# Optimization experiments

Hardware: AMD Instinct MI355X
Metric: run time of the kernel (lower is better)

Reference implementation:

```python
import jax, jax.numpy as jnp
import numpy as np

EPS = 1e-5

def _layernorm(x, w, b):
    # x: [B, L, C]; WithBias_LayerNorm over last dim (biased variance)
    mu = jnp.mean(x, axis=-1, keepdims=True)
    var = jnp.mean((x - mu) ** 2, axis=-1, keepdims=True)
    return (x - mu) / jnp.sqrt(var + EPS) * w + b

def _selective_scan(x, x_proj_w, dt_w, A_logs, Ds):
    # x: [B, D, L]  (D = ssm d_inner = 192, N = d_state = 16, R = dt_rank = 6)
    Bsz, D, L = x.shape
    N = A_logs.shape[1]
    R = dt_w.shape[1]
    x_dbl = jnp.einsum('bdl,rd->blr', x, x_proj_w)            # [B, L, R+2N]
    dts_r = x_dbl[..., :R]
    Bs = x_dbl[..., R:R + N]                                   # [B, L, N]
    Cs = x_dbl[..., R + N:]                                    # [B, L, N]
    dts = jax.nn.softplus(jnp.einsum('blr,dr->bld', dts_r, dt_w))  # [B, L, D]
    As = -jnp.exp(A_logs.astype(jnp.float32))                  # [D, N]
    dt_A = jnp.exp(jnp.einsum('bld,dn->bldn', dts, As))        # [B, L, D, N]
    dt_B_x = jnp.einsum('bld,bln,bdl->bldn', dts, Bs, x)       # [B, L, D, N]

    def step(u, inp):
        a, bx, c = inp                                         # [B,D,N],[B,D,N],[B,N]
        u = a * u + bx
        y = jnp.einsum('bdn,bn->bd', u, c)
        return u, y

    u0 = jnp.zeros((Bsz, D, N), dtype=jnp.float32)
    _, ys = jax.lax.scan(step, u0, (jnp.swapaxes(dt_A, 0, 1),
                                     jnp.swapaxes(dt_B_x, 0, 1),
                                     jnp.swapaxes(Cs, 0, 1)))
    y = jnp.swapaxes(ys, 0, 1)                                 # [B, L, D]
    y = y + jnp.einsum('bdl,d->bld', x, Ds.astype(jnp.float32))
    return y


def setup_inputs() -> dict:
    key = jax.random.key(0)
    ks = jax.random.split(key, 12)
    B, C, H, W = 64, 2048, 24, 8
    D_in2, Dssm, N, R = 384, 192, 16, 6
    s = 0.02
    return {
        'feat_map': jax.random.normal(ks[0], (B, C, H, W), jnp.float32),
        'ln_w': jnp.ones((C,), jnp.float32),
        'ln_b': jnp.zeros((C,), jnp.float32),
        'in_w': jax.random.normal(ks[1], (D_in2, C), jnp.float32) * s,
        'in_b': jnp.zeros((D_in2,), jnp.float32),
        'x_proj_w': jax.random.normal(ks[2], (R + 2 * N, Dssm), jnp.float32) * s,
        'dt_w': jax.random.normal(ks[3], (Dssm, R), jnp.float32) * 0.1,
        'A_logs': jnp.log(jnp.broadcast_to(jnp.arange(1, N + 1, dtype=jnp.float32), (Dssm, N))),
        'Ds': jnp.ones((Dssm,), jnp.float32),
        'out_w': jax.random.normal(ks[4], (C, Dssm), jnp.float32) * s,
        'out_b': jnp.zeros((C,), jnp.float32),
        'mo_w': jax.random.normal(ks[5], (C, C), jnp.float32) * s,
        'mo_b': jnp.zeros((C,), jnp.float32),
        'bn_w': jnp.ones((C,), jnp.float32),
        'bn_b': jnp.zeros((C,), jnp.float32),
        'bn_rm': jax.random.normal(ks[6], (C,), jnp.float32) * 0.1,
        'bn_rv': jax.random.uniform(ks[7], (C,), jnp.float32) + 0.5,
    }


def reference(feat_map, ln_w, ln_b, in_w, in_b, x_proj_w, dt_w, A_logs, Ds,
              out_w, out_b, mo_w, mo_b, bn_w, bn_b, bn_rm, bn_rv):
    B, C, H, W = feat_map.shape
    L = H * W
    x3 = feat_map.transpose(0, 2, 3, 1).reshape(B, L, C)       # to_3d
    fm = _layernorm(x3, ln_w, ln_b)                            # normalized feat_map [B, L, C]
    xz = jnp.einsum('blc,oc->blo', fm, in_w) + in_b            # 1x1 conv in_proj
    x, z = jnp.split(xz, 2, axis=-1)                           # each [B, L, 192]
    xd = jnp.swapaxes(x, 1, 2)                                 # [B, D, L]
    yf = _selective_scan(xd, x_proj_w, dt_w, A_logs, Ds)       # [B, L, D]
    yb = _selective_scan(xd[:, :, ::-1], x_proj_w, dt_w, A_logs, Ds)[:, ::-1, :]
    ssm = yf + yb                                              # [B, L, D]
    ssm = ssm * jax.nn.silu(z)
    out = jnp.einsum('bld,cd->blc', ssm, out_w) + out_b        # out_proj 1x1 conv
    out = out + fm                                             # drop_path is identity at eval
    out = jnp.einsum('blc,oc->blo', out, mo_w) + mo_b          # mamba_out conv 1x1
    out = (out - bn_rm) / jnp.sqrt(bn_rv + EPS) * bn_w + bn_b  # BatchNorm (eval)
    out = jax.nn.relu(out)
    return out.reshape(B, H, W, C).transpose(0, 3, 1, 2)
```

## Files before the change

kernel.cpp:

```cpp
#include <hip/hip_runtime.h>
#include <math.h>

#define EPSV 1e-5f


typedef __attribute__((ext_vector_type(8))) __bf16 bf16x8;
typedef __attribute__((ext_vector_type(4))) float f32x4;

__device__ __forceinline__ ushort f2bf(float f) {
  union { float f; unsigned u; } v; v.f = f;
  const unsigned r = v.u + 0x7fffu + ((v.u >> 16) & 1u);
  return (ushort)(r >> 16);
}

#define GLOAD16(G, L) __builtin_amdgcn_global_load_lds( \
    (__attribute__((address_space(1))) void*)(G), \
    (__attribute__((address_space(3))) void*)(L), 16, 0, 0)

#define BAR() do { asm volatile("" ::: "memory"); \
  __builtin_amdgcn_s_barrier(); \
  asm volatile("" ::: "memory"); } while (0)

template<int CTRL>
__device__ __forceinline__ float dpp_add(float y) {
  const int s = __builtin_amdgcn_update_dpp(0, __float_as_int(y), CTRL, 0xF, 0xF, true);
  return y + __int_as_float(s);
}
__device__ __forceinline__ float reduce16(float y) {
  y = dpp_add<0xB1>(y);
  y = dpp_add<0x4E>(y);
  y = dpp_add<0x124>(y);
  y = dpp_add<0x128>(y);
  return y;
}

__global__ __launch_bounds__(256) void cvt_kernel(
    const float* __restrict__ s, ushort* __restrict__ d, int n)
{
  const int i = (blockIdx.x * 256 + threadIdx.x) * 4;
  if (i + 3 < n) {
    const float4 v = *(const float4*)(s + i);
    ushort4 o;
    o.x = f2bf(v.x); o.y = f2bf(v.y); o.z = f2bf(v.z); o.w = f2bf(v.w);
    *(ushort4*)(d + i) = o;
  }
}

__global__ __launch_bounds__(256) void transpose_w(
    const float* __restrict__ w, ushort* __restrict__ wT)
{
  __shared__ float t[64][65];
  const int c0 = blockIdx.x * 64, d0 = blockIdx.y * 64;
  const int tl = threadIdx.x & 63, tg = threadIdx.x >> 6;
#pragma unroll
  for (int r = 0; r < 16; ++r) {
    const int c = r * 4 + tg;
    t[c][tl] = w[(size_t)(c0 + c) * 192 + d0 + tl];
  }
  __syncthreads();
#pragma unroll
  for (int r = 0; r < 16; ++r) {
    const int d = r * 4 + tg;
    wT[(size_t)(d0 + d) * 2048 + c0 + tl] = f2bf(t[tl][d]);
  }
}

__global__ __launch_bounds__(256) void ln_stats(
    const float* __restrict__ feat, float* __restrict__ sums)
{
  const int b = blockIdx.x, c0 = blockIdx.y * 128;
  const int l = threadIdx.x;
  if (l >= 192) return;
  const float* p = feat + ((size_t)b * 2048 + c0) * 192 + l;
  float s = 0.f, sq = 0.f;
  for (int c = 0; c < 128; ++c) { const float v = p[(size_t)c * 192]; s += v; sq = fmaf(v, v, sq); }
  atomicAdd(&sums[(b * 192 + l) * 2], s);
  atomicAdd(&sums[(b * 192 + l) * 2 + 1], sq);
}

__global__ __launch_bounds__(256) void ln_apply(
    const float* __restrict__ feat, const float* __restrict__ sums,
    const float* __restrict__ lnw, const float* __restrict__ lnb,
    ushort* __restrict__ fm)
{
  __shared__ float tile[64][65];
  __shared__ float smu[64], srs[64];
  const int b = blockIdx.x, c0 = blockIdx.y * 64, l0 = blockIdx.z * 64;
  const int tl = threadIdx.x & 63, tg = threadIdx.x >> 6;
#pragma unroll
  for (int r = 0; r < 16; ++r) {
    const int c = r * 4 + tg;
    tile[c][tl] = feat[((size_t)b * 2048 + c0 + c) * 192 + l0 + tl];
  }
  if (threadIdx.x < 64) {
    const float s  = sums[(b * 192 + l0 + threadIdx.x) * 2];
    const float sq = sums[(b * 192 + l0 + threadIdx.x) * 2 + 1];
    const float mu = s * (1.f / 2048.f);
    smu[threadIdx.x] = mu;
    srs[threadIdx.x] = rsqrtf(sq * (1.f / 2048.f) - mu * mu + EPSV);
  }
  __syncthreads();
  const float w = lnw[c0 + tl], bb = lnb[c0 + tl];
#pragma unroll
  for (int r = 0; r < 16; ++r) {
    const int ll = r * 4 + tg;
    fm[((size_t)(b * 192 + l0 + ll)) * 2048 + c0 + tl] =
        f2bf((tile[tl][ll] - smu[ll]) * srs[ll] * w + bb);
  }
}

__device__ __forceinline__ void mfma_phase(
    const ushort* __restrict__ Ag, int lda,
    const ushort* __restrict__ Bg, int ldb, int K,
    int bm, int bn, int tid, ushort* As, ushort* Bs, f32x4 acc[4][4])
{
  const int lane = tid & 63, wave = tid >> 6;
  const int wm = (wave & 1) << 6, wn = (wave >> 1) << 6;
  const int fr = lane & 15, q = lane >> 4;
  const int r0 = tid >> 2, kc = (tid & 3) << 3;
  const int lb = (tid & 192) * 8;
  for (int k0 = 0; k0 < K; k0 += 32) {
    __syncthreads();
    GLOAD16(Ag + (size_t)(bm + r0) * lda + k0 + kc,      As + lb);
    GLOAD16(Ag + (size_t)(bm + 64 + r0) * lda + k0 + kc, As + 2048 + lb);
    GLOAD16(Bg + (size_t)(bn + r0) * ldb + k0 + kc,      Bs + lb);
    GLOAD16(Bg + (size_t)(bn + 64 + r0) * ldb + k0 + kc, Bs + 2048 + lb);
    __syncthreads();
    bf16x8 af[4], bfr[4];
#pragma unroll
    for (int i = 0; i < 4; ++i) {
      af[i]  = *(const bf16x8*)&As[(wm + i * 16 + fr) * 32 + q * 8];
      bfr[i] = *(const bf16x8*)&Bs[(wn + i * 16 + fr) * 32 + q * 8];
    }
#pragma unroll
    for (int i = 0; i < 4; ++i)
#pragma unroll
      for (int j = 0; j < 4; ++j)
        acc[i][j] = __builtin_amdgcn_mfma_f32_16x16x32_bf16(af[i], bfr[j], acc[i][j], 0, 0, 0);
  }
}

__global__ __launch_bounds__(256) void mfma_gemm0(
    const ushort* __restrict__ A1, const ushort* __restrict__ B1,
    const float* __restrict__ p0, float* __restrict__ out)
{
  __shared__ ushort As[4096], Bs[4096];
  const int tid = threadIdx.x;
  const int bm = blockIdx.y * 128, bn = blockIdx.x * 128;
  f32x4 acc[4][4];
#pragma unroll
  for (int i = 0; i < 4; ++i)
#pragma unroll
    for (int j = 0; j < 4; ++j) acc[i][j] = (f32x4)(0.f);

  mfma_phase(A1, 2048, B1, 2048, 2048, bm, bn, tid, As, Bs, acc);

  const int lane = tid & 63, wave = tid >> 6;
  const int wm = (wave & 1) << 6, wn = (wave >> 1) << 6;
  const int fr = lane & 15, q = lane >> 4;
#pragma unroll
  for (int mi = 0; mi < 4; ++mi) {
    const int m0 = bm + wm + mi * 16 + q * 4;
#pragma unroll
    for (int ni = 0; ni < 4; ++ni) {
      const int n = bn + wn + ni * 16 + fr;
      const float bias = p0[n];
#pragma unroll
      for (int r = 0; r < 4; ++r)
        out[(size_t)(m0 + r) * 384 + n] = acc[mi][ni][r] + bias;
    }
  }
}

__global__ __launch_bounds__(256) void w2_partial(
    const ushort* __restrict__ A1, const ushort* __restrict__ B1,
    float* __restrict__ part)
{
  __shared__ ushort As[4096], Bs[4096];
  const int tid = threadIdx.x;
  const int bm = blockIdx.y * 128, bn = blockIdx.x * 128;
  const int kz = blockIdx.z * 256;
  f32x4 acc[4][4];
#pragma unroll
  for (int i = 0; i < 4; ++i)
#pragma unroll
    for (int j = 0; j < 4; ++j) acc[i][j] = (f32x4)(0.f);

  mfma_phase(A1 + kz, 2048, B1 + kz, 2048, 256, bm, bn, tid, As, Bs, acc);

  const int lane = tid & 63, wave = tid >> 6;
  const int wm = (wave & 1) << 6, wn = (wave >> 1) << 6;
  const int fr = lane & 15, q = lane >> 4;
  float* pout = part + (size_t)blockIdx.z * 2048 * 256;
#pragma unroll
  for (int mi = 0; mi < 4; ++mi) {
    const int m0 = bm + wm + mi * 16 + q * 4;
#pragma unroll
    for (int ni = 0; ni < 4; ++ni) {
      const int n = bn + wn + ni * 16 + fr;
#pragma unroll
      for (int r = 0; r < 4; ++r)
        pout[(size_t)(m0 + r) * 256 + n] = acc[mi][ni][r];
    }
  }
}

__global__ __launch_bounds__(256) void w2_reduce(
    const float* __restrict__ part, ushort* __restrict__ W2b)
{
  const int i = blockIdx.x * 256 + threadIdx.x;
  const float4* p4 = (const float4*)part;
  float4 s = p4[i];
#pragma unroll
  for (int z = 1; z < 8; ++z) {
    const float4 v = p4[i + z * 131072];
    s.x += v.x; s.y += v.y; s.z += v.z; s.w += v.w;
  }
  ushort4 o;
  o.x = f2bf(s.x); o.y = f2bf(s.y); o.z = f2bf(s.z); o.w = f2bf(s.w);
  *(ushort4*)(W2b + (size_t)i * 4) = o;
}

__device__ __forceinline__ void stage_half(
    int t, int kind,
    int bm, int bn, int tid,
    const ushort* __restrict__ fmw, const ushort* __restrict__ mow,
    const ushort* __restrict__ ssmb, const ushort* __restrict__ w2b,
    ushort* As, ushort* Bs)
{
  const bool isA = (kind < 2);
  const ushort* G; int ld, k0;
  if (t < 32) { G = isA ? fmw : mow;  ld = 2048; k0 = t * 64; }
  else        { G = isA ? ssmb : w2b; ld = 256;  k0 = (t - 32) * 64; }
  const int p0 = isA ? bm : bn;
  ushort* L = (isA ? As : Bs) + (t & 1) * 16384 + (kind & 1) * 8192;
  const int w = tid >> 6, l = tid & 63;
#pragma unroll
  for (int j = 0; j < 2; ++j) {
    const int LC = j * 512 + w * 64 + l;
    const int row = (kind & 1) * 128 + (LC >> 3);
    const int sc = (LC & 7) ^ (row & 7);
    GLOAD16(G + (size_t)(p0 + row) * ld + k0 + sc * 8, L + j * 4096 + w * 512);
  }
}

__global__ __launch_bounds__(512, 2) void mfma_gemm_big(
    const ushort* __restrict__ fmw,  const ushort* __restrict__ mow,
    const ushort* __restrict__ ssmb, const ushort* __restrict__ w2b,
    const float* __restrict__ scale, const float* __restrict__ shift,
    float* __restrict__ out)
{
  __shared__ ushort As[2 * 16384];
  __shared__ ushort Bs[2 * 16384];
  const int tid = threadIdx.x;
  const int flat = blockIdx.x;
  const int bx = flat & 7, by = flat >> 3;
  const int bm = by * 256, bn = bx * 256;

  const int lane = tid & 63, wave = tid >> 6;
  const int wr = wave >> 2, wc = wave & 3;
  const int fr = lane & 15, q = lane >> 4;

  constexpr int NT = 36;

  f32x4 acc[8][4];
#pragma unroll
  for (int i = 0; i < 8; ++i)
#pragma unroll
    for (int j = 0; j < 4; ++j) acc[i][j] = (f32x4)(0.f);

  stage_half(0, 0, bm, bn, tid, fmw, mow, ssmb, w2b, As, Bs);
  stage_half(0, 1, bm, bn, tid, fmw, mow, ssmb, w2b, As, Bs);
  stage_half(0, 2, bm, bn, tid, fmw, mow, ssmb, w2b, As, Bs);
  stage_half(0, 3, bm, bn, tid, fmw, mow, ssmb, w2b, As, Bs);
  stage_half(1, 2, bm, bn, tid, fmw, mow, ssmb, w2b, As, Bs);
  stage_half(1, 3, bm, bn, tid, fmw, mow, ssmb, w2b, As, Bs);
  asm volatile("s_waitcnt vmcnt(4)" ::: "memory");
  BAR();

  for (int t = 0; t < NT; ++t) {
    const ushort* Ab = As + (t & 1) * 16384;
    const ushort* Bb = Bs + (t & 1) * 16384;
    bf16x8 bfr[4];
#pragma unroll
    for (int ph = 0; ph < 4; ++ph) {
      const int ks = ph >> 1, mh = ph & 1;
      const int kswz = (((ks << 2) + q) ^ (fr & 7)) << 3;
      bf16x8 af[4];
#pragma unroll
      for (int mi = 0; mi < 4; ++mi)
        af[mi] = *(const bf16x8*)&Ab[(wr * 128 + mh * 64 + mi * 16 + fr) * 64 + kswz];
      if (mh == 0) {
#pragma unroll
        for (int ni = 0; ni < 4; ++ni)
          bfr[ni] = *(const bf16x8*)&Bb[(wc * 64 + ni * 16 + fr) * 64 + kswz];
      }
      if (ph == 0) {
        if (t + 1 < NT) {
          stage_half(t + 1, 0, bm, bn, tid, fmw, mow, ssmb, w2b, As, Bs);
          stage_half(t + 1, 1, bm, bn, tid, fmw, mow, ssmb, w2b, As, Bs);
        }
      } else if (ph == 3) {
        if (t + 2 < NT) {
          stage_half(t + 2, 2, bm, bn, tid, fmw, mow, ssmb, w2b, As, Bs);
          stage_half(t + 2, 3, bm, bn, tid, fmw, mow, ssmb, w2b, As, Bs);
        }
      }
      BAR();
      __builtin_amdgcn_s_setprio(1);
#pragma unroll
      for (int mi = 0; mi < 4; ++mi)
#pragma unroll
        for (int ni = 0; ni < 4; ++ni)
          acc[mh * 4 + mi][ni] = __builtin_amdgcn_mfma_f32_16x16x32_bf16(
              af[mi], bfr[ni], acc[mh * 4 + mi][ni], 0, 0, 0);
      __builtin_amdgcn_s_setprio(0);
      if (ph == 3) {
        if (t <= 33) asm volatile("s_waitcnt vmcnt(4)" ::: "memory");
        else if (t == 34) asm volatile("s_waitcnt vmcnt(0)" ::: "memory");
      }
      BAR();
    }
  }

#pragma unroll
  for (int mi = 0; mi < 8; ++mi) {
    const int m0 = bm + wr * 128 + mi * 16 + q * 4;
    const int b = m0 / 192, l0 = m0 - b * 192;
#pragma unroll
    for (int ni = 0; ni < 4; ++ni) {
      const int n = bn + wc * 64 + ni * 16 + fr;
      const float sc = scale[n], sh = shift[n];
      float4 o;
      o.x = fmaxf(fmaf(acc[mi][ni][0], sc, sh), 0.f);
      o.y = fmaxf(fmaf(acc[mi][ni][1], sc, sh), 0.f);
      o.z = fmaxf(fmaf(acc[mi][ni][2], sc, sh), 0.f);
      o.w = fmaxf(fmaf(acc[mi][ni][3], sc, sh), 0.f);
      *(float4*)(out + ((size_t)b * 2048 + n) * 192 + l0) = o;
    }
  }
}

__global__ __launch_bounds__(64) void xproj_kernel(
    const float* __restrict__ xz, const float* __restrict__ xpw,
    const float* __restrict__ dtw, float* __restrict__ dts,
    float* __restrict__ Bsb, float* __restrict__ Csb)
{
  const int m = blockIdx.x, tid = threadIdx.x;
  __shared__ float xrow[192];
  __shared__ float xdbl[38];
  const float* src = xz + (size_t)m * 384;
#pragma unroll
  for (int i = 0; i < 3; ++i) xrow[tid + i * 64] = src[tid + i * 64];
  __syncthreads();
  if (tid < 38) {
    float a = 0.f;
    const float* wr = xpw + tid * 192;
    for (int d = 0; d < 192; ++d) a = fmaf(xrow[d], wr[d], a);
    xdbl[tid] = a;
  }
  __syncthreads();
  if (tid < 16) Bsb[(size_t)m * 16 + tid] = xdbl[6 + tid];
  else if (tid < 32) Csb[(size_t)m * 16 + (tid - 16)] = xdbl[22 + (tid - 16)];
#pragma unroll
  for (int i = 0; i < 3; ++i) {
    const int d = tid + i * 64;
    const float* w = dtw + d * 6;
    float a = xdbl[0] * w[0] + xdbl[1] * w[1] + xdbl[2] * w[2]
            + xdbl[3] * w[3] + xdbl[4] * w[4] + xdbl[5] * w[5];
    dts[(size_t)m * 192 + d] = (a > 20.f) ? a : log1pf(__expf(a));
  }
}

__global__ __launch_bounds__(256) void scan_kernel(
    const float* __restrict__ xz, const float* __restrict__ dts,
    const float* __restrict__ Bsb, const float* __restrict__ Csb,
    const float* __restrict__ A_logs, const float* __restrict__ Ds,
    ushort* __restrict__ ssm)
{
  __shared__ float s_dt[16 * 196], s_x[16 * 196], s_B[16 * 196],
                   s_C[16 * 196], s_y[16 * 196];
  const int tid = threadIdx.x;
  const int b = blockIdx.x / 12, dblk = blockIdx.x - b * 12;
  const int d0 = dblk * 16;
  const size_t rbase = (size_t)b * 192;
  for (int i = tid; i < 768; i += 256) {
    const int l = i >> 2, j = (i & 3) << 2;
    const size_t row = rbase + l;
    const float4 dtv = *(const float4*)(dts + row * 192 + d0 + j);
    const float4 xv  = *(const float4*)(xz  + row * 384 + d0 + j);
    const float4 Bv  = *(const float4*)(Bsb + row * 16 + j);
    const float4 Cv  = *(const float4*)(Csb + row * 16 + j);
    s_dt[(j + 0) * 196 + l] = dtv.x; s_dt[(j + 1) * 196 + l] = dtv.y;
    s_dt[(j + 2) * 196 + l] = dtv.z; s_dt[(j + 3) * 196 + l] = dtv.w;
    s_x [(j + 0) * 196 + l] = xv.x;  s_x [(j + 1) * 196 + l] = xv.y;
    s_x [(j + 2) * 196 + l] = xv.z;  s_x [(j + 3) * 196 + l] = xv.w;
    s_B [(j + 0) * 196 + l] = Bv.x;  s_B [(j + 1) * 196 + l] = Bv.y;
    s_B [(j + 2) * 196 + l] = Bv.z;  s_B [(j + 3) * 196 + l] = Bv.w;
    s_C [(j + 0) * 196 + l] = Cv.x;  s_C [(j + 1) * 196 + l] = Cv.y;
    s_C [(j + 2) * 196 + l] = Cv.z;  s_C [(j + 3) * 196 + l] = Cv.w;
  }
  __syncthreads();
  const int n = tid & 15, dl = tid >> 4;
  const float Acoef = -expf(A_logs[(d0 + dl) * 16 + n]);
  const float* pdt = s_dt + dl * 196;
  const float* px  = s_x  + dl * 196;
  const float* pB  = s_B  + n * 196;
  const float* pC  = s_C  + n * 196;
  float* py = s_y + dl * 196;
  float u = 0.f;
  for (int l0 = 0; l0 < 192; l0 += 4) {
    const float4 dtv = *(const float4*)(pdt + l0);
    const float4 xv  = *(const float4*)(px + l0);
    const float4 Bv  = *(const float4*)(pB + l0);
    const float4 Cv  = *(const float4*)(pC + l0);
    u = fmaf(__expf(dtv.x * Acoef), u, dtv.x * Bv.x * xv.x);
    { float y = reduce16(u * Cv.x); if (n == 0) py[l0 + 0] = y; }
    u = fmaf(__expf(dtv.y * Acoef), u, dtv.y * Bv.y * xv.y);
    { float y = reduce16(u * Cv.y); if (n == 0) py[l0 + 1] = y; }
    u = fmaf(__expf(dtv.z * Acoef), u, dtv.z * Bv.z * xv.z);
    { float y = reduce16(u * Cv.z); if (n == 0) py[l0 + 2] = y; }
    u = fmaf(__expf(dtv.w * Acoef), u, dtv.w * Bv.w * xv.w);
    { float y = reduce16(u * Cv.w); if (n == 0) py[l0 + 3] = y; }
  }
  u = 0.f;
  for (int l0 = 188; l0 >= 0; l0 -= 4) {
    const float4 dtv = *(const float4*)(pdt + l0);
    const float4 xv  = *(const float4*)(px + l0);
    const float4 Bv  = *(const float4*)(pB + l0);
    const float4 Cv  = *(const float4*)(pC + l0);
    u = fmaf(__expf(dtv.w * Acoef), u, dtv.w * Bv.w * xv.w);
    { float y = reduce16(u * Cv.w); if (n == 0) py[l0 + 3] += y; }
    u = fmaf(__expf(dtv.z * Acoef), u, dtv.z * Bv.z * xv.z);
    { float y = reduce16(u * Cv.z); if (n == 0) py[l0 + 2] += y; }
    u = fmaf(__expf(dtv.y * Acoef), u, dtv.y * Bv.y * xv.y);
    { float y = reduce16(u * Cv.y); if (n == 0) py[l0 + 1] += y; }
    u = fmaf(__expf(dtv.x * Acoef), u, dtv.x * Bv.x * xv.x);
    { float y = reduce16(u * Cv.x); if (n == 0) py[l0 + 0] += y; }
  }
  __syncthreads();
  for (int i = tid; i < 768; i += 256) {
    const int l = i >> 2, j = (i & 3) << 2;
    const size_t row = rbase + l;
    float4 y4, x4;
    y4.x = s_y[(j + 0) * 196 + l]; y4.y = s_y[(j + 1) * 196 + l];
    y4.z = s_y[(j + 2) * 196 + l]; y4.w = s_y[(j + 3) * 196 + l];
    x4.x = s_x[(j + 0) * 196 + l]; x4.y = s_x[(j + 1) * 196 + l];
    x4.z = s_x[(j + 2) * 196 + l]; x4.w = s_x[(j + 3) * 196 + l];
    const float4 z4 = *(const float4*)(xz + row * 384 + 192 + d0 + j);
    const float4 D4 = *(const float4*)(Ds + d0 + j);
    ushort4 o;
    o.x = f2bf((y4.x + 2.f * x4.x * D4.x) * (z4.x / (1.f + __expf(-z4.x))));
    o.y = f2bf((y4.y + 2.f * x4.y * D4.y) * (z4.y / (1.f + __expf(-z4.y))));
    o.z = f2bf((y4.z + 2.f * x4.z * D4.z) * (z4.z / (1.f + __expf(-z4.z))));
    o.w = f2bf((y4.w + 2.f * x4.w * D4.w) * (z4.w / (1.f + __expf(-z4.w))));
    *(ushort4*)(ssm + row * 256 + d0 + j) = o;
  }
}

__global__ __launch_bounds__(64) void prep_kernel(
    const float* __restrict__ mo_w, const float* __restrict__ mo_b,
    const float* __restrict__ out_b,
    const float* __restrict__ bn_w, const float* __restrict__ bn_b,
    const float* __restrict__ bn_rm, const float* __restrict__ bn_rv,
    float* __restrict__ scale, float* __restrict__ shift)
{
  const int o = blockIdx.x, tid = threadIdx.x;
  float s = 0.f;
  for (int c = tid; c < 2048; c += 64) s = fmaf(mo_w[(size_t)o * 2048 + c], out_b[c], s);
#pragma unroll
  for (int off = 32; off > 0; off >>= 1) s += __shfl_down(s, off, 64);
  if (tid == 0) {
    const float b2 = s + mo_b[o];
    const float sc = bn_w[o] * rsqrtf(bn_rv[o] + EPSV);
    scale[o] = sc;
    shift[o] = (b2 - bn_rm[o]) * sc + bn_b[o];
  }
}

extern "C" void kernel_launch(void* const* d_in, const int* in_sizes, int n_in,
                              void* d_out, int out_size, void* d_ws, size_t ws_size,
                              hipStream_t stream) {
  const float* feat  = (const float*)d_in[0];
  const float* ln_w  = (const float*)d_in[1];
  const float* ln_b  = (const float*)d_in[2];
  const float* in_w  = (const float*)d_in[3];
  const float* in_b  = (const float*)d_in[4];
  const float* xpw   = (const float*)d_in[5];
  const float* dtw   = (const float*)d_in[6];
  const float* A_logs= (const float*)d_in[7];
  const float* Ds    = (const float*)d_in[8];
  const float* out_w = (const float*)d_in[9];
  const float* out_b = (const float*)d_in[10];
  const float* mo_w  = (const float*)d_in[11];
  const float* mo_b  = (const float*)d_in[12];
  const float* bn_w  = (const float*)d_in[13];
  const float* bn_b  = (const float*)d_in[14];
  const float* bn_rm = (const float*)d_in[15];
  const float* bn_rv = (const float*)d_in[16];
  float* out = (float*)d_out;

  uint8_t* p = (uint8_t*)d_ws;
  ushort* fm_b  = (ushort*)p; p += (size_t)12288 * 2048 * 2;
  float*  xz    = (float*)p;  p += (size_t)12288 * 384 * 4;
  float*  dts   = (float*)p;  p += (size_t)12288 * 192 * 4;
  float*  Bsb   = (float*)p;  p += (size_t)12288 * 16 * 4;
  float*  Csb   = (float*)p;  p += (size_t)12288 * 16 * 4;
  ushort* ssm_b = (ushort*)p; p += (size_t)12288 * 256 * 2;
  ushort* W2b   = (ushort*)p; p += (size_t)2048 * 256 * 2;
  ushort* owT_b = (ushort*)p; p += (size_t)256 * 2048 * 2;
  ushort* mo_wb = (ushort*)p; p += (size_t)2048 * 2048 * 2;
  ushort* in_wb = (ushort*)p; p += (size_t)384 * 2048 * 2;
  float*  scale = (float*)p;  p += 2048 * 4;
  float*  shift = (float*)p;  p += 2048 * 4;
  float*  sums  = (float*)p;  p += (size_t)64 * 192 * 2 * 4;
  if ((size_t)(p - (uint8_t*)d_ws) > ws_size) return;
  float* W2part = xz;

  cvt_kernel<<<4096, 256, 0, stream>>>(mo_w, mo_wb, 2048 * 2048);
  cvt_kernel<<<768, 256, 0, stream>>>(in_w, in_wb, 384 * 2048);
  hipMemsetAsync(owT_b, 0, (size_t)256 * 2048 * 2, stream);
  hipMemsetAsync(ssm_b, 0, (size_t)12288 * 256 * 2, stream);
  transpose_w<<<dim3(32, 3), 256, 0, stream>>>(out_w, owT_b);

  hipMemsetAsync(sums, 0, (size_t)64 * 192 * 2 * 4, stream);
  ln_stats<<<dim3(64, 16), 256, 0, stream>>>(feat, sums);
  ln_apply<<<dim3(64, 32, 3), 256, 0, stream>>>(feat, sums, ln_w, ln_b, fm_b);

  mfma_gemm0<<<dim3(3, 96), 256, 0, stream>>>(fm_b, in_wb, in_b, xz);

  xproj_kernel<<<12288, 64, 0, stream>>>(xz, xpw, dtw, dts, Bsb, Csb);
  scan_kernel<<<768, 256, 0, stream>>>(xz, dts, Bsb, Csb, A_logs, Ds, ssm_b);

  w2_partial<<<dim3(2, 16, 8), 256, 0, stream>>>(mo_wb, owT_b, W2part);
  w2_reduce<<<512, 256, 0, stream>>>(W2part, W2b);
  prep_kernel<<<2048, 64, 0, stream>>>(mo_w, mo_b, out_b, bn_w, bn_b, bn_rm, bn_rv, scale, shift);

  mfma_gemm_big<<<384, 512, 0, stream>>>(fm_b, mo_wb, ssm_b, W2b, scale, shift, out);
}
```

Before: 598.0 us.

## Replace in_proj GEMM with double-buffered swizzled 256x128 kernel; remap big GEMM blocks per XCD

The simple 128x128 in_proj GEMM, which issued a load and then synchronised every K step, is replaced by a 512-thread 256x128 tile kernel. It uses swizzled LDS, prefetches two stages ahead and interleaves MFMA with global-to-LDS loads. The big fused GEMM now maps block indices so that each XCD works on a contiguous band of rows, aiming for better L2 reuse. Its A-stage loads are also split across two phases to spread out memory issue. The cost is higher register and LDS use and fewer blocks (144) for the in_proj GEMM.

```diff
diff --git a/kernel.cpp b/kernel.cpp
--- a/kernel.cpp
+++ b/kernel.cpp
@@ -140,38 +140,6 @@
   }
 }
 
-__global__ __launch_bounds__(256) void mfma_gemm0(
-    const ushort* __restrict__ A1, const ushort* __restrict__ B1,
-    const float* __restrict__ p0, float* __restrict__ out)
-{
-  __shared__ ushort As[4096], Bs[4096];
-  const int tid = threadIdx.x;
-  const int bm = blockIdx.y * 128, bn = blockIdx.x * 128;
-  f32x4 acc[4][4];
-#pragma unroll
-  for (int i = 0; i < 4; ++i)
-#pragma unroll
-    for (int j = 0; j < 4; ++j) acc[i][j] = (f32x4)(0.f);
-
-  mfma_phase(A1, 2048, B1, 2048, 2048, bm, bn, tid, As, Bs, acc);
-
-  const int lane = tid & 63, wave = tid >> 6;
-  const int wm = (wave & 1) << 6, wn = (wave >> 1) << 6;
-  const int fr = lane & 15, q = lane >> 4;
-#pragma unroll
-  for (int mi = 0; mi < 4; ++mi) {
-    const int m0 = bm + wm + mi * 16 + q * 4;
-#pragma unroll
-    for (int ni = 0; ni < 4; ++ni) {
-      const int n = bn + wn + ni * 16 + fr;
-      const float bias = p0[n];
-#pragma unroll
-      for (int r = 0; r < 4; ++r)
-        out[(size_t)(m0 + r) * 384 + n] = acc[mi][ni][r] + bias;
-    }
-  }
-}
-
 __global__ __launch_bounds__(256) void w2_partial(
     const ushort* __restrict__ A1, const ushort* __restrict__ B1,
     float* __restrict__ part)
@@ -219,6 +187,114 @@
   ushort4 o;
   o.x = f2bf(s.x); o.y = f2bf(s.y); o.z = f2bf(s.z); o.w = f2bf(s.w);
   *(ushort4*)(W2b + (size_t)i * 4) = o;
+}
+
+__device__ __forceinline__ void g0_stage_A(
+    int t, int kind, int bm, int tid, const ushort* __restrict__ fmw, ushort* As)
+{
+  ushort* L = As + (t & 1) * 16384 + kind * 8192;
+  const int w = tid >> 6, l = tid & 63;
+#pragma unroll
+  for (int j = 0; j < 2; ++j) {
+    const int LC = j * 512 + w * 64 + l;
+    const int row = kind * 128 + (LC >> 3);
+    const int sc = (LC & 7) ^ (row & 7);
+    GLOAD16(fmw + (size_t)(bm + row) * 2048 + t * 64 + sc * 8, L + j * 4096 + w * 512);
+  }
+}
+__device__ __forceinline__ void g0_stage_B(
+    int t, int bn, int tid, const ushort* __restrict__ Bw, ushort* Bs)
+{
+  ushort* L = Bs + (t & 1) * 8192;
+  const int w = tid >> 6, l = tid & 63;
+#pragma unroll
+  for (int j = 0; j < 2; ++j) {
+    const int LC = j * 512 + w * 64 + l;
+    const int row = LC >> 3;
+    const int sc = (LC & 7) ^ (row & 7);
+    GLOAD16(Bw + (size_t)(bn + row) * 2048 + t * 64 + sc * 8, L + j * 4096 + w * 512);
+  }
+}
+
+__global__ __launch_bounds__(512, 2) void mfma_gemm0_big(
+    const ushort* __restrict__ fmw, const ushort* __restrict__ inw,
+    const float* __restrict__ bias, float* __restrict__ out)
+{
+  __shared__ ushort As[2 * 16384];
+  __shared__ ushort Bs[2 * 8192];
+  const int tid = threadIdx.x;
+  const int bm = blockIdx.y * 256, bn = blockIdx.x * 128;
+  const int lane = tid & 63, wave = tid >> 6;
+  const int wr = wave >> 1, wc = wave & 1;
+  const int fr = lane & 15, q = lane >> 4;
+  constexpr int NT = 32;
+
+  f32x4 acc[4][4];
+#pragma unroll
+  for (int i = 0; i < 4; ++i)
+#pragma unroll
+    for (int j = 0; j < 4; ++j) acc[i][j] = (f32x4)(0.f);
+
+  g0_stage_A(0, 0, bm, tid, fmw, As);
+  g0_stage_A(0, 1, bm, tid, fmw, As);
+  g0_stage_B(0, bn, tid, inw, Bs);
+  g0_stage_B(1, bn, tid, inw, Bs);
+  asm volatile("s_waitcnt vmcnt(2)" ::: "memory");
+  BAR();
+
+  for (int t = 0; t < NT; ++t) {
+    const ushort* Ab = As + (t & 1) * 16384;
+    const ushort* Bb = Bs + (t & 1) * 8192;
+    bf16x8 bfr[4];
+#pragma unroll
+    for (int ph = 0; ph < 4; ++ph) {
+      const int ks = ph >> 1, mh = ph & 1;
+      const int kswz = (((ks << 2) + q) ^ (fr & 7)) << 3;
+      bf16x8 af[2];
+#pragma unroll
+      for (int mi = 0; mi < 2; ++mi)
+        af[mi] = *(const bf16x8*)&Ab[(wr * 64 + mh * 32 + mi * 16 + fr) * 64 + kswz];
+      if (mh == 0) {
+#pragma unroll
+        for (int ni = 0; ni < 4; ++ni)
+          bfr[ni] = *(const bf16x8*)&Bb[(wc * 64 + ni * 16 + fr) * 64 + kswz];
+      }
+      if (ph == 0) {
+        if (t + 1 < NT) g0_stage_A(t + 1, 0, bm, tid, fmw, As);
+      } else if (ph == 1) {
+        if (t + 1 < NT) g0_stage_A(t + 1, 1, bm, tid, fmw, As);
+      } else if (ph == 3) {
+        if (t + 2 < NT) g0_stage_B(t + 2, bn, tid, inw, Bs);
+      }
+      BAR();
+      __builtin_amdgcn_s_setprio(1);
+#pragma unroll
+      for (int mi = 0; mi < 2; ++mi)
+#pragma unroll
+        for (int ni = 0; ni < 4; ++ni)
+          acc[mh * 2 + mi][ni] = __builtin_amdgcn_mfma_f32_16x16x32_bf16(
+              af[mi], bfr[ni], acc[mh * 2 + mi][ni], 0, 0, 0);
+      __builtin_amdgcn_s_setprio(0);
+      if (ph == 3) {
+        if (t <= NT - 3) asm volatile("s_waitcnt vmcnt(2)" ::: "memory");
+        else if (t == NT - 2) asm volatile("s_waitcnt vmcnt(0)" ::: "memory");
+      }
+      BAR();
+    }
+  }
+
+#pragma unroll
+  for (int a = 0; a < 4; ++a) {
+    const int m0 = bm + wr * 64 + a * 16 + q * 4;
+#pragma unroll
+    for (int ni = 0; ni < 4; ++ni) {
+      const int n = bn + wc * 64 + ni * 16 + fr;
+      const float bb = bias[n];
+#pragma unroll
+      for (int r = 0; r < 4; ++r)
+        out[(size_t)(m0 + r) * 384 + n] = acc[a][ni][r] + bb;
+    }
+  }
 }
 
 __device__ __forceinline__ void stage_half(
@@ -254,8 +330,9 @@
   __shared__ ushort Bs[2 * 16384];
   const int tid = threadIdx.x;
   const int flat = blockIdx.x;
-  const int bx = flat & 7, by = flat >> 3;
-  const int bm = by * 256, bn = bx * 256;
+  const int xcd = flat & 7, j = flat >> 3;
+  const int by = xcd * 6 + (j >> 3);
+  const int bm = by * 256, bn = (j & 7) * 256;
 
   const int lane = tid & 63, wave = tid >> 6;
   const int wr = wave >> 2, wc = wave & 3;
@@ -267,7 +344,7 @@
 #pragma unroll
   for (int i = 0; i < 8; ++i)
 #pragma unroll
-    for (int j = 0; j < 4; ++j) acc[i][j] = (f32x4)(0.f);
+    for (int j2 = 0; j2 < 4; ++j2) acc[i][j2] = (f32x4)(0.f);
 
   stage_half(0, 0, bm, bn, tid, fmw, mow, ssmb, w2b, As, Bs);
   stage_half(0, 1, bm, bn, tid, fmw, mow, ssmb, w2b, As, Bs);
@@ -296,10 +373,9 @@
           bfr[ni] = *(const bf16x8*)&Bb[(wc * 64 + ni * 16 + fr) * 64 + kswz];
       }
       if (ph == 0) {
-        if (t + 1 < NT) {
-          stage_half(t + 1, 0, bm, bn, tid, fmw, mow, ssmb, w2b, As, Bs);
-          stage_half(t + 1, 1, bm, bn, tid, fmw, mow, ssmb, w2b, As, Bs);
-        }
+        if (t + 1 < NT) stage_half(t + 1, 0, bm, bn, tid, fmw, mow, ssmb, w2b, As, Bs);
+      } else if (ph == 1) {
+        if (t + 1 < NT) stage_half(t + 1, 1, bm, bn, tid, fmw, mow, ssmb, w2b, As, Bs);
       } else if (ph == 3) {
         if (t + 2 < NT) {
           stage_half(t + 2, 2, bm, bn, tid, fmw, mow, ssmb, w2b, As, Bs);
@@ -527,7 +603,7 @@
   ln_stats<<<dim3(64, 16), 256, 0, stream>>>(feat, sums);
   ln_apply<<<dim3(64, 32, 3), 256, 0, stream>>>(feat, sums, ln_w, ln_b, fm_b);
 
-  mfma_gemm0<<<dim3(3, 96), 256, 0, stream>>>(fm_b, in_wb, in_b, xz);
+  mfma_gemm0_big<<<dim3(3, 48), 512, 0, stream>>>(fm_b, in_wb, in_b, xz);
 
   xproj_kernel<<<12288, 64, 0, stream>>>(xz, xpw, dtw, dts, Bsb, Csb);
   scan_kernel<<<768, 256, 0, stream>>>(xz, dts, Bsb, Csb, A_logs, Ds, ssm_b);
```

Measured after the change: 586.0 us. -2.0%, faster.
